# Kernel tuning notes

Measured on AMD Instinct MI355X. Metric: run time of the kernel, lower is better.

## Reference

```python
import jax, jax.numpy as jnp
import numpy as np


def setup_inputs() -> dict:
    key = jax.random.key(0)
    k1, k2 = jax.random.split(key)
    # probabilities strictly inside (0,1) so log(x) and log(1-x) are finite
    input = jax.random.uniform(k1, (16384, 4096), dtype=jnp.float32) * 0.98 + 0.01
    target = jax.random.randint(k2, (16384, 4096), 0, 2, dtype=jnp.int32)
    return {"input": input, "target": target}


def reference(input, target):
    x = input.reshape(-1)
    t = target.reshape(-1)
    n = x.shape[0]                      # static Python int
    tf = t.astype(x.dtype)
    s = tf.sum()                        # number of positives
    length = jnp.asarray(n + 1, x.dtype)
    wp = length / (s + 1)               # positive-class weight
    wn = length / (length - s)          # negative-class weight
    # fused masked elementwise + reduction (targets not in {0,1} contribute 0)
    pos = jnp.where(t == 1, -jnp.log(x), jnp.zeros((), x.dtype)).sum()
    neg = jnp.where(t == 0, -jnp.log1p(-x), jnp.zeros((), x.dtype)).sum()
    loss = ((wp + 1) * pos + (wn + 1) * neg) / n
    return loss
```

## Files before the change

kernel.cpp:

```cpp
#include <hip/hip_runtime.h>

#define BLOCK 256
#define GRID 2048
#define UNROLL 8

__global__ __launch_bounds__(BLOCK) void wbce_reduce_kernel(
    const float* __restrict__ x, const int* __restrict__ t,
    long long n, double* __restrict__ ws) {
    const int n4 = (int)(n >> 2);
    const int tid = threadIdx.x;

    const int per_iter = BLOCK * UNROLL;
    const int iters_total = n4 / (GRID * per_iter);
    const int main_count = GRID * per_iter * iters_total;

    float tot = 0.0f, pos = 0.0f;
    int cnt = 0;

    const float4* __restrict__ x4 = (const float4*)x;
    const int4*   __restrict__ t4 = (const int4*)t;

#define PROC(XC, TC)                                        \
    {                                                       \
        float xi = (XC); int ti = (TC);                     \
        float a = ti ? xi : (1.0f - xi);                    \
        float v = -__log2f(a);                              \
        tot += v;                                           \
        pos += ti ? v : 0.0f;                               \
        cnt += ti;                                          \
    }

    int base = blockIdx.x * per_iter * iters_total + tid;
    for (int it = 0; it < iters_total; ++it, base += per_iter) {
        float4 xv[UNROLL];
        int4   tv[UNROLL];
#pragma unroll
        for (int j = 0; j < UNROLL; ++j)
            xv[j] = x4[base + j * BLOCK];
#pragma unroll
        for (int j = 0; j < UNROLL; ++j)
            tv[j] = t4[base + j * BLOCK];
#pragma unroll
        for (int j = 0; j < UNROLL; ++j) {
            PROC(xv[j].x, tv[j].x)
            PROC(xv[j].y, tv[j].y)
            PROC(xv[j].z, tv[j].z)
            PROC(xv[j].w, tv[j].w)
        }
    }

    for (int i = main_count + blockIdx.x * BLOCK + tid; i < n4; i += GRID * BLOCK) {
        float4 xv = x4[i];
        int4   tv = t4[i];
        PROC(xv.x, tv.x)
        PROC(xv.y, tv.y)
        PROC(xv.z, tv.z)
        PROC(xv.w, tv.w)
    }

    if (blockIdx.x == 0 && tid == 0) {
        for (long long i = (long long)n4 << 2; i < n; ++i) {
            float xi = x[i]; int ti = t[i];
            float a = ti ? xi : (1.0f - xi);
            float v = -__log2f(a);
            tot += v;
            pos += ti ? v : 0.0f;
            cnt += ti;
        }
    }
#undef PROC

    float neg = tot - pos;

    for (int o = 32; o > 0; o >>= 1) {
        pos += __shfl_down(pos, o);
        neg += __shfl_down(neg, o);
        cnt += __shfl_down(cnt, o);
    }

    __shared__ float s_pos[BLOCK / 64];
    __shared__ float s_neg[BLOCK / 64];
    __shared__ int   s_cnt[BLOCK / 64];
    const int lane = tid & 63;
    const int wave = tid >> 6;
    if (lane == 0) {
        s_pos[wave] = pos;
        s_neg[wave] = neg;
        s_cnt[wave] = cnt;
    }
    __syncthreads();

    if (tid == 0) {
        double bpos = 0.0, bneg = 0.0;
        long long bcnt = 0;
        for (int w = 0; w < BLOCK / 64; ++w) {
            bpos += (double)s_pos[w];
            bneg += (double)s_neg[w];
            bcnt += s_cnt[w];
        }
        atomicAdd(&ws[0], (double)bcnt);
        atomicAdd(&ws[1], bpos);
        atomicAdd(&ws[2], bneg);
    }
}

__global__ void wbce_finalize_kernel(const double* __restrict__ ws,
                                     float* __restrict__ out, double n) {
    const double LN2 = 0.6931471805599453;
    double s   = ws[0];
    double pos = ws[1] * LN2;
    double neg = ws[2] * LN2;
    double len = n + 1.0;
    double wp  = len / (s + 1.0);
    double wn  = len / (len - s);
    double loss = ((wp + 1.0) * pos + (wn + 1.0) * neg) / n;
    out[0] = (float)loss;
}

extern "C" void kernel_launch(void* const* d_in, const int* in_sizes, int n_in,
                              void* d_out, int out_size, void* d_ws, size_t ws_size,
                              hipStream_t stream) {
    const float* x = (const float*)d_in[0];
    const int*   t = (const int*)d_in[1];
    float* out = (float*)d_out;
    double* ws = (double*)d_ws;
    const long long n = (long long)in_sizes[0];

    hipMemsetAsync(ws, 0, 3 * sizeof(double), stream);
    wbce_reduce_kernel<<<GRID, BLOCK, 0, stream>>>(x, t, n, ws);
    wbce_finalize_kernel<<<1, 1, 0, stream>>>(ws, out, (double)n);
}
```

Baseline: 142.0 us.

## Stream inputs through LDS with double-buffered global_load_lds per wave

Replaces the register-unrolled float4/int4 loads with a per-wave, two-slot LDS pipeline that uses the global_load_lds builtin and explicit vmcnt waits, so the next stage's loads are in flight while the current one is processed. Each wave now walks a contiguous chunk of its own instead of a block-strided pattern. The log negation moves into the finalize kernel to save one op per element. Only one 16-byte load per lane is in flight per stage, which gives less memory-level parallelism than the previous 8-deep unroll, and the extra LDS round-trip and waitcnt stalls add cost.

```diff
diff --git a/kernel.cpp b/kernel.cpp
--- a/kernel.cpp
+++ b/kernel.cpp
@@ -1,74 +1,102 @@
 #include <hip/hip_runtime.h>
 
 #define BLOCK 256
-#define GRID 2048
-#define UNROLL 8
+#define GRID  2048
+#define NWAVE (BLOCK / 64)
 
-__global__ __launch_bounds__(BLOCK) void wbce_reduce_kernel(
-    const float* __restrict__ x, const int* __restrict__ t,
-    long long n, double* __restrict__ ws) {
-    const int n4 = (int)(n >> 2);
-    const int tid = threadIdx.x;
-
-    const int per_iter = BLOCK * UNROLL;
-    const int iters_total = n4 / (GRID * per_iter);
-    const int main_count = GRID * per_iter * iters_total;
-
-    float tot = 0.0f, pos = 0.0f;
-    int cnt = 0;
-
-    const float4* __restrict__ x4 = (const float4*)x;
-    const int4*   __restrict__ t4 = (const int4*)t;
+#define AS3P(p) ((__attribute__((address_space(3))) void*)(p))
+#define AS1P(p) ((const __attribute__((address_space(1))) void*)(p))
 
 #define PROC(XC, TC)                                        \
     {                                                       \
         float xi = (XC); int ti = (TC);                     \
         float a = ti ? xi : (1.0f - xi);                    \
-        float v = -__log2f(a);                              \
+        float v = __log2f(a);    \
         tot += v;                                           \
         pos += ti ? v : 0.0f;                               \
         cnt += ti;                                          \
     }
 
-    int base = blockIdx.x * per_iter * iters_total + tid;
-    for (int it = 0; it < iters_total; ++it, base += per_iter) {
-        float4 xv[UNROLL];
-        int4   tv[UNROLL];
-#pragma unroll
-        for (int j = 0; j < UNROLL; ++j)
-            xv[j] = x4[base + j * BLOCK];
-#pragma unroll
-        for (int j = 0; j < UNROLL; ++j)
-            tv[j] = t4[base + j * BLOCK];
-#pragma unroll
-        for (int j = 0; j < UNROLL; ++j) {
-            PROC(xv[j].x, tv[j].x)
-            PROC(xv[j].y, tv[j].y)
-            PROC(xv[j].z, tv[j].z)
-            PROC(xv[j].w, tv[j].w)
+#define PROC4(xv, tv) \
+    PROC(xv.x, tv.x) PROC(xv.y, tv.y) PROC(xv.z, tv.z) PROC(xv.w, tv.w)
+
+__global__ __launch_bounds__(BLOCK) void wbce_reduce_kernel(
+    const float* __restrict__ x, const int* __restrict__ t,
+    long long n, double* __restrict__ ws) {
+    const int tid  = threadIdx.x;
+    const int lane = tid & 63;
+    const int wv   = tid >> 6;
+
+    const long long n4 = n >> 2;
+    const long long waves_total = (long long)GRID * NWAVE;
+    const int nst = (int)(n4 / (waves_total * 64));
+    const long long main_f4 = waves_total * 64 * (long long)nst;
+
+    float tot = 0.0f, pos = 0.0f;
+    int cnt = 0;
+
+    __shared__ float4 sx [NWAVE][2][64];
+    __shared__ int4   stl[NWAVE][2][64];
+
+    if (nst >= 2) {
+        const int wid = blockIdx.x * NWAVE + wv;
+        const long long wbase = (long long)wid * 64 * nst;
+        const float4* gxs = ((const float4*)x) + wbase + lane;
+        const int4*   gts = ((const int4*)t)   + wbase + lane;
+
+#define ISSUE_STAGE(STG, SLOT) do {                                          \
+        __builtin_amdgcn_global_load_lds(AS1P(gxs + (long long)(STG) * 64),  \
+                                         AS3P(&sx[wv][SLOT][0]), 16, 0, 0);  \
+        __builtin_amdgcn_global_load_lds(AS1P(gts + (long long)(STG) * 64),  \
+                                         AS3P(&stl[wv][SLOT][0]), 16, 0, 0); \
+    } while (0)
+
+        ISSUE_STAGE(0, 0);
+        ISSUE_STAGE(1, 1);
+
+        for (int stg = 0; stg < nst; ++stg) {
+            const int slot = stg & 1;
+            if (stg < nst - 1) {
+                asm volatile("s_waitcnt vmcnt(2)" ::: "memory");
+            } else {
+                asm volatile("s_waitcnt vmcnt(0)" ::: "memory");
+            }
+            __builtin_amdgcn_sched_barrier(0);
+
+            float4 xv = sx[wv][slot][lane];
+            int4   tv = stl[wv][slot][lane];
+
+            asm volatile("s_waitcnt lgkmcnt(0)" ::: "memory");
+            __builtin_amdgcn_sched_barrier(0);
+
+            if (stg + 2 < nst) ISSUE_STAGE(stg + 2, slot);
+
+            PROC4(xv, tv)
+        }
+#undef ISSUE_STAGE
+    }
+
+    {
+        const float4* __restrict__ x4 = (const float4*)x;
+        const int4*   __restrict__ t4 = (const int4*)t;
+        for (long long i = main_f4 + (long long)blockIdx.x * BLOCK + tid;
+             i < n4; i += (long long)GRID * BLOCK) {
+            float4 xv = x4[i];
+            int4   tv = t4[i];
+            PROC4(xv, tv)
         }
     }
 
-    for (int i = main_count + blockIdx.x * BLOCK + tid; i < n4; i += GRID * BLOCK) {
-        float4 xv = x4[i];
-        int4   tv = t4[i];
-        PROC(xv.x, tv.x)
-        PROC(xv.y, tv.y)
-        PROC(xv.z, tv.z)
-        PROC(xv.w, tv.w)
-    }
-
     if (blockIdx.x == 0 && tid == 0) {
-        for (long long i = (long long)n4 << 2; i < n; ++i) {
+        for (long long i = n4 << 2; i < n; ++i) {
             float xi = x[i]; int ti = t[i];
             float a = ti ? xi : (1.0f - xi);
-            float v = -__log2f(a);
+            float v = __log2f(a);
             tot += v;
             pos += ti ? v : 0.0f;
             cnt += ti;
         }
     }
-#undef PROC
 
     float neg = tot - pos;
 
@@ -78,22 +106,20 @@
         cnt += __shfl_down(cnt, o);
     }
 
-    __shared__ float s_pos[BLOCK / 64];
-    __shared__ float s_neg[BLOCK / 64];
-    __shared__ int   s_cnt[BLOCK / 64];
-    const int lane = tid & 63;
-    const int wave = tid >> 6;
+    __shared__ float s_pos[NWAVE];
+    __shared__ float s_neg[NWAVE];
+    __shared__ int   s_cnt[NWAVE];
     if (lane == 0) {
-        s_pos[wave] = pos;
-        s_neg[wave] = neg;
-        s_cnt[wave] = cnt;
+        s_pos[wv] = pos;
+        s_neg[wv] = neg;
+        s_cnt[wv] = cnt;
     }
     __syncthreads();
 
     if (tid == 0) {
         double bpos = 0.0, bneg = 0.0;
         long long bcnt = 0;
-        for (int w = 0; w < BLOCK / 64; ++w) {
+        for (int w = 0; w < NWAVE; ++w) {
             bpos += (double)s_pos[w];
             bneg += (double)s_neg[w];
             bcnt += s_cnt[w];
@@ -108,8 +134,8 @@
                                      float* __restrict__ out, double n) {
     const double LN2 = 0.6931471805599453;
     double s   = ws[0];
-    double pos = ws[1] * LN2;
-    double neg = ws[2] * LN2;
+    double pos = -ws[1] * LN2;
+    double neg = -ws[2] * LN2;
     double len = n + 1.0;
     double wp  = len / (s + 1.0);
     double wn  = len / (len - s);
```

After: 158.3 us. 11.5% more time.
